# Kernel tuning notes

Measured on AMD Instinct MI355X. Metric: run time of the kernel, lower is better.

Reference implementation:

```python
import jax, jax.numpy as jnp
import numpy as np
from math import sqrt

N_HEADS = 16

def setup_inputs() -> dict:
    key = jax.random.key(0)
    ks = jax.random.split(key, 6)
    B, T, C = 4, 2048, 1024
    s = 0.02
    return {
        "X": jax.random.normal(ks[0], (B, T, C), jnp.float32),
        "Wq": jax.random.normal(ks[1], (C, C), jnp.float32) * s,
        "Wk": jax.random.normal(ks[2], (C, C), jnp.float32) * s,
        "Wv": jax.random.normal(ks[3], (C, C), jnp.float32) * s,
        "Wo": jax.random.normal(ks[4], (C, C), jnp.float32) * s,
        "bo": jnp.zeros((C,), jnp.float32),
    }

def reference(X, Wq, Wk, Wv, Wo, bo):
    B, T, C = X.shape
    H = N_HEADS
    D = C // H
    scale = sqrt(C / H)  # == sqrt(D)
    # Linear layers (torch Linear: y = x @ W.T), split into heads: [B,H,T,D]
    Q = (X @ Wq.T).reshape(B, T, H, D).transpose(0, 2, 1, 3)
    K = (X @ Wk.T).reshape(B, T, H, D).transpose(0, 2, 1, 3)
    V = (X @ Wv.T).reshape(B, T, H, D).transpose(0, 2, 1, 3)
    A = jnp.einsum("bhtd,bhsd->bhts", Q, K) / scale  # [B,H,T,T]
    causal = jnp.tril(jnp.ones((T, T), dtype=bool))
    A = jnp.where(causal, A, -jnp.inf)
    A = jax.nn.softmax(A, axis=-1)
    Y = jnp.einsum("bhts,bhsd->bhtd", A, V)  # [B,H,T,D]
    Y = Y.transpose(0, 2, 1, 3).reshape(B, T, C)
    return Y @ Wo.T + bo
```

## Files before the change

kernel.cpp:

```cpp
#include <hip/hip_runtime.h>
#include <hip/hip_bf16.h>
#include <stdint.h>


typedef unsigned short u16;
typedef __attribute__((ext_vector_type(8))) __bf16 bf16x8;
typedef __attribute__((ext_vector_type(4))) float  f32x4;
typedef __attribute__((ext_vector_type(4))) unsigned short u16x4;
typedef __attribute__((ext_vector_type(8))) unsigned short u16x8;
typedef __attribute__((ext_vector_type(4))) short s16x4;

#define B_  4
#define T_  2048
#define C_  1024
#define H_  16
#define D_  64
#define BT_ (B_ * T_)
#define NT_ 16

#define Q_SCALE 0.1803368801111204f

__device__ __forceinline__ u16 f32_to_bf16(float f) {
    unsigned int u = __float_as_uint(f);
    unsigned int r = (u + 0x7FFFu + ((u >> 16) & 1u)) >> 16;
    return (u16)r;
}

__device__ __forceinline__ unsigned int pk_bf16(float a, float b) {
    float2 f2; f2.x = a; f2.y = b;
    __hip_bfloat162 h = __float22bfloat162_rn(f2);
    return *(unsigned int*)&h;
}

__device__ __forceinline__ void async16(const void* g, void* lds) {
    __builtin_amdgcn_global_load_lds(
        (const __attribute__((address_space(1))) void*)g,
        (__attribute__((address_space(3))) void*)lds, 16, 0, 0);
}

__global__ void cast_all_kernel(const float* __restrict__ X,
                                const float* __restrict__ w0, const float* __restrict__ w1,
                                const float* __restrict__ w2, const float* __restrict__ w3,
                                u16* __restrict__ xo,
                                u16* __restrict__ o0, u16* __restrict__ o1,
                                u16* __restrict__ o2, u16* __restrict__ o3) {
    int id = blockIdx.x;
    const float* in; u16* out; int i;
    if (id < 8192) {
        in = X; out = xo; i = id * 256 + threadIdx.x;
    } else {
        int k = (id - 8192) >> 10;
        in  = (k == 0) ? w0 : (k == 1) ? w1 : (k == 2) ? w2 : w3;
        out = (k == 0) ? o0 : (k == 1) ? o1 : (k == 2) ? o2 : o3;
        i = ((id - 8192) & 1023) * 256 + threadIdx.x;
    }
    float4 v = ((const float4*)in)[i];
    u16x4 o;
    o[0] = f32_to_bf16(v.x); o[1] = f32_to_bf16(v.y);
    o[2] = f32_to_bf16(v.z); o[3] = f32_to_bf16(v.w);
    ((u16x4*)out)[i] = o;
}

#define QPHASE(CB, MH, NH, DOISSUE, G, GATE)                                      \
  {                                                                               \
    if ((NH) == 0) {                                                              \
      _Pragma("unroll")                                                           \
      for (int f = 0; f < 4; ++f) {                                               \
        _Pragma("unroll")                                                         \
        for (int ks = 0; ks < 2; ++ks)                                            \
          xf[f][ks] = *(const bf16x8*)((CB) + (MH) * 16384 + axoff[f][ks]);       \
      }                                                                           \
    }                                                                             \
    if ((MH) == 0) {                                                              \
      _Pragma("unroll")                                                           \
      for (int e = 0; e < 2; ++e) {                                               \
        _Pragma("unroll")                                                         \
        for (int ks = 0; ks < 2; ++ks)                                            \
          wf[NH][e][ks] = *(const bf16x8*)((CB) + (NH) * 16384 + bwoff[e][ks]);   \
      }                                                                           \
    }                                                                             \
    if (DOISSUE) issue_unit(G);                                                   \
    if ((GATE) == 4)      asm volatile("s_waitcnt vmcnt(4)" ::: "memory");        \
    else if ((GATE) == 2) asm volatile("s_waitcnt vmcnt(2)" ::: "memory");        \
    else if ((GATE) == 0) asm volatile("s_waitcnt vmcnt(0)" ::: "memory");        \
    __builtin_amdgcn_s_barrier();                                                 \
    asm volatile("" ::: "memory");                                                \
    __builtin_amdgcn_s_setprio(1);                                                \
    _Pragma("unroll")                                                             \
    for (int f = 0; f < 4; ++f) {                                                 \
      _Pragma("unroll")                                                           \
      for (int e = 0; e < 2; ++e) {                                               \
        f32x4 a_ = acc[(MH) * 4 + f][(NH) * 2 + e];                               \
        a_ = __builtin_amdgcn_mfma_f32_16x16x32_bf16(wf[NH][e][0], xf[f][0], a_, 0, 0, 0); \
        a_ = __builtin_amdgcn_mfma_f32_16x16x32_bf16(wf[NH][e][1], xf[f][1], a_, 0, 0, 0); \
        acc[(MH) * 4 + f][(NH) * 2 + e] = a_;                                     \
      }                                                                           \
    }                                                                             \
    __builtin_amdgcn_s_setprio(0);                                                \
    asm volatile("" ::: "memory");                                                \
    __builtin_amdgcn_s_barrier();                                                 \
    asm volatile("" ::: "memory");                                                \
  }

__device__ __forceinline__ void qkv256_core(const u16* __restrict__ Arow,
                                            const u16* __restrict__ Brow,
                                            char* lds, f32x4 (&acc)[8][4])
{
    int tid = threadIdx.x, lane = tid & 63, w = tid >> 6;
    int quad = lane >> 4, l15 = lane & 15;
    int wm = w >> 2, wn = w & 3;

    int gc = (((tid & 7) - (tid >> 3)) & 7) * 8;
    const u16* xsrc0 = Arow + (size_t)(tid >> 3) * C_ + gc;
    const u16* xsrc1 = xsrc0 + (size_t)64 * C_;
    const u16* wsrc0 = Brow + (size_t)(tid >> 3) * C_ + gc;
    const u16* wsrc1 = wsrc0 + (size_t)64 * C_;

    auto issue_unit = [&](int g) {
        int u = g & 3, kt = g >> 2;
        char* d = lds + ((kt & 1) << 16) + (u << 14) + (w << 10);
        size_t off = (size_t)(u & 1) * (128 * C_) + (size_t)kt * 64;
        const u16* s0 = (u < 2) ? xsrc0 : wsrc0;
        const u16* s1 = (u < 2) ? xsrc1 : wsrc1;
        async16(s0 + off, d);
        async16(s1 + off, d + 8192);
    };

    int axoff[4][2], bwoff[2][2];
#pragma unroll
    for (int f = 0; f < 4; ++f) {
        int r = wm * 64 + f * 16 + l15;
#pragma unroll
        for (int ks = 0; ks < 2; ++ks)
            axoff[f][ks] = r * 128 + (((ks * 4 + quad + r) & 7) << 4);
    }
#pragma unroll
    for (int e = 0; e < 2; ++e) {
        int r = wn * 32 + e * 16 + l15;
#pragma unroll
        for (int ks = 0; ks < 2; ++ks)
            bwoff[e][ks] = 32768 + r * 128 + (((ks * 4 + quad + r) & 7) << 4);
    }

    bf16x8 xf[4][2];
    bf16x8 wf[2][2][2];

    issue_unit(0); issue_unit(2); issue_unit(3); issue_unit(1);
    asm volatile("s_waitcnt vmcnt(4)" ::: "memory");
    __builtin_amdgcn_s_barrier();
    asm volatile("" ::: "memory");

    for (int t = 0; t < NT_ - 1; ++t) {
        char* cb = lds + ((t & 1) << 16);
        int g4 = (t + 1) << 2;
        QPHASE(cb, 0, 0, 1, g4 + 0, 4);
        QPHASE(cb, 0, 1, 1, g4 + 2, 4);
        QPHASE(cb, 1, 0, 1, g4 + 3, -1);
        QPHASE(cb, 1, 1, 1, g4 + 1, 4);
    }
    {
        char* cb = lds + 65536;
        QPHASE(cb, 0, 0, 0, 0, 2);
        QPHASE(cb, 0, 1, 0, 0, 0);
        QPHASE(cb, 1, 0, 0, 0, -1);
        QPHASE(cb, 1, 1, 0, 0, -1);
    }
}

__device__ __forceinline__ void qkv128v_core(const u16* __restrict__ Arow,
                                             const u16* __restrict__ Brow,
                                             char* lds, f32x4 (&acc)[4][4])
{
    int tid = threadIdx.x, lane = tid & 63, w = tid >> 6;
    int quad = lane >> 4, l15 = lane & 15;
    int wm = w >> 2, wn = w & 3;

    int gc = (((tid & 7) - (tid >> 3)) & 7) * 8;
    const u16* asrc  = Arow + (size_t)(tid >> 3) * C_ + gc;
    const u16* bsrc0 = Brow + (size_t)(tid >> 3) * C_ + gc;
    const u16* bsrc1 = bsrc0 + (size_t)64 * C_;

    auto issue3 = [&](int kt) {
        char* db = lds + ((kt & 1) << 16) + (w << 10);
        int ko = kt * 64;
        async16(asrc + ko,                       db);
        async16(asrc + ko + (size_t)64 * C_,     db + 8192);
        async16(bsrc0 + ko,                      db + 32768);
        async16(bsrc1 + ko,                      db + 32768 + 8192);
        async16(bsrc0 + ko + (size_t)128 * C_,   db + 49152);
        async16(bsrc1 + ko + (size_t)128 * C_,   db + 49152 + 8192);
    };

    int axoff[4][2], bwoff[2][2];
#pragma unroll
    for (int f = 0; f < 4; ++f) {
        int r = wm * 64 + f * 16 + l15;
#pragma unroll
        for (int ks = 0; ks < 2; ++ks)
            axoff[f][ks] = r * 128 + (((ks * 4 + quad + r) & 7) << 4);
    }
#pragma unroll
    for (int e = 0; e < 2; ++e) {
        int r = wn * 32 + e * 16 + l15;
#pragma unroll
        for (int ks = 0; ks < 2; ++ks)
            bwoff[e][ks] = 32768 + r * 128 + (((ks * 4 + quad + r) & 7) << 4);
    }

    bf16x8 xf[4][2], wf[2][2];

    issue3(0);

    for (int t = 0; t < NT_; ++t) {
        char* cb = lds + ((t & 1) << 16);
        if (t + 1 < NT_) issue3(t + 1);
        if (t == NT_ - 1) asm volatile("s_waitcnt vmcnt(0)" ::: "memory");
        else              asm volatile("s_waitcnt vmcnt(6)" ::: "memory");
        __builtin_amdgcn_s_barrier();
        asm volatile("" ::: "memory");

#pragma unroll
        for (int f = 0; f < 4; ++f)
#pragma unroll
            for (int ks = 0; ks < 2; ++ks)
                xf[f][ks] = *(const bf16x8*)(cb + axoff[f][ks]);
#pragma unroll
        for (int e = 0; e < 2; ++e)
#pragma unroll
            for (int ks = 0; ks < 2; ++ks)
                wf[e][ks] = *(const bf16x8*)(cb + bwoff[e][ks]);
        __builtin_amdgcn_s_setprio(1);
#pragma unroll
        for (int f = 0; f < 4; ++f)
#pragma unroll
            for (int e = 0; e < 2; ++e) {
                f32x4 a_ = acc[f][e];
                a_ = __builtin_amdgcn_mfma_f32_16x16x32_bf16(xf[f][0], wf[e][0], a_, 0, 0, 0);
                a_ = __builtin_amdgcn_mfma_f32_16x16x32_bf16(xf[f][1], wf[e][1], a_, 0, 0, 0);
                acc[f][e] = a_;
            }
        __builtin_amdgcn_s_setprio(0);

#pragma unroll
        for (int e = 0; e < 2; ++e)
#pragma unroll
            for (int ks = 0; ks < 2; ++ks)
                wf[e][ks] = *(const bf16x8*)(cb + 16384 + bwoff[e][ks]);
        __builtin_amdgcn_s_setprio(1);
#pragma unroll
        for (int f = 0; f < 4; ++f)
#pragma unroll
            for (int e = 0; e < 2; ++e) {
                f32x4 a_ = acc[f][2 + e];
                a_ = __builtin_amdgcn_mfma_f32_16x16x32_bf16(xf[f][0], wf[e][0], a_, 0, 0, 0);
                a_ = __builtin_amdgcn_mfma_f32_16x16x32_bf16(xf[f][1], wf[e][1], a_, 0, 0, 0);
                acc[f][2 + e] = a_;
            }
        __builtin_amdgcn_s_setprio(0);
        asm volatile("" ::: "memory");
        __builtin_amdgcn_s_barrier();
        asm volatile("" ::: "memory");
    }
}

__global__ __launch_bounds__(512, 2) void qkv_mix512(
    const u16* __restrict__ Xb, const u16* __restrict__ Wcat,
    u16* __restrict__ Qb, u16* __restrict__ Kb, u16* __restrict__ Vtb)
{
    __shared__ __attribute__((aligned(128))) char LDSRAW[131072];

    int id = blockIdx.x;
    int tid = threadIdx.x, lane = tid & 63, w = tid >> 6;
    int quad = lane >> 4, l15 = lane & 15;
    int wm = w >> 2, wn = w & 3;

    if (id < 256) {
        int ti = (id & 7) * 32 + (id >> 3);
        int bm = ti & 31, bn = ti >> 5;
        int m0 = bm * 256, chb = bn * 256;

        f32x4 acc[8][4];
        const f32x4 z4 = {0.f, 0.f, 0.f, 0.f};
#pragma unroll
        for (int i = 0; i < 8; ++i)
#pragma unroll
            for (int j = 0; j < 4; ++j) acc[i][j] = z4;

        qkv256_core(Xb + (size_t)m0 * C_, Wcat + (size_t)chb * C_, LDSRAW, acc);

#pragma unroll
        for (int mi = 0; mi < 8; ++mi) {
            size_t trow = (size_t)(m0 + (mi >> 2) * 128 + wm * 64 + (mi & 3) * 16 + l15) * C_;
#pragma unroll
            for (int nj = 0; nj < 4; ++nj) {
                int colb = chb + (nj >> 1) * 128 + wn * 32 + (nj & 1) * 16 + quad * 4;
                u16* OUT = (colb < 1024) ? Qb : Kb;
                float sc = (colb < 1024) ? Q_SCALE : 1.0f;
                u16x4 v;
#pragma unroll
                for (int rr = 0; rr < 4; ++rr) v[rr] = f32_to_bf16(acc[mi][nj][rr] * sc);
                *(u16x4*)&OUT[trow + (colb & 1023)] = v;
            }
        }
    } else {
        int id2 = id - 256;
        int hw = (id2 & 7) * 32 + (id2 >> 3);
        int vt = hw >> 6;
        int bm = (hw & 63) >> 1, half = hw & 1;
        int m0h = bm * 256 + half * 128;
        int chb = 2048 + vt * 256;

        f32x4 acc[4][4];
        const f32x4 z4 = {0.f, 0.f, 0.f, 0.f};
#pragma unroll
        for (int i = 0; i < 4; ++i)
#pragma unroll
            for (int j = 0; j < 4; ++j) acc[i][j] = z4;

        qkv128v_core(Xb + (size_t)m0h * C_, Wcat + (size_t)chb * C_, LDSRAW, acc);

#pragma unroll
        for (int mi = 0; mi < 4; ++mi) {
            int t0 = m0h + wm * 64 + mi * 16 + quad * 4;
            int b_ = t0 >> 11, tl = t0 & (T_ - 1);
#pragma unroll
            for (int nj = 0; nj < 4; ++nj) {
                int ch = chb + (nj >> 1) * 128 + wn * 32 + (nj & 1) * 16 + l15;
                int h = (ch >> 6) & 15, d = ch & 63;
                u16x4 v;
#pragma unroll
                for (int rr = 0; rr < 4; ++rr) v[rr] = f32_to_bf16(acc[mi][nj][rr]);
                *(u16x4*)&Vtb[((size_t)(b_ * H_ + h) * D_ + d) * T_ + tl] = v;
            }
        }
    }
}

#define RD8(CB, KS, FX, FW)                                                      \
    _Pragma("unroll") for (int i_ = 0; i_ < 4; ++i_) {                           \
        FX[i_] = *(const bf16x8*)((CB) + (KS) * 8192  + xoff[i_]);               \
        FW[i_] = *(const bf16x8*)((CB) + (KS) * 16384 + woff[i_]);               \
    }

#define PPH(ISSUE, GATE, FX, FW, ...)                                            \
  {                                                                              \
    ISSUE;                                                                       \
    if ((GATE) == 6)      asm volatile("s_waitcnt vmcnt(6)" ::: "memory");       \
    else if ((GATE) == 3) asm volatile("s_waitcnt vmcnt(3)" ::: "memory");       \
    else if ((GATE) == 0) asm volatile("s_waitcnt vmcnt(0)" ::: "memory");       \
    __builtin_amdgcn_s_barrier();                                                \
    asm volatile("" ::: "memory");                                               \
    __VA_ARGS__;                                                                 \
    __builtin_amdgcn_sched_barrier(0);                                           \
    __builtin_amdgcn_s_setprio(1);                                               \
    _Pragma("unroll") for (int i = 0; i < 4; ++i)                                \
      _Pragma("unroll") for (int j = 0; j < 4; ++j)                              \
        acc[i][j] = __builtin_amdgcn_mfma_f32_16x16x32_bf16(FW[j], FX[i], acc[i][j], 0, 0, 0); \
    __builtin_amdgcn_s_setprio(0);                                               \
    asm volatile("" ::: "memory");                                               \
    __builtin_amdgcn_s_barrier();                                                \
    asm volatile("" ::: "memory");                                               \
  }

__device__ __forceinline__ void gemm8p_core(const u16* __restrict__ Arow,
                                            const u16* __restrict__ Brow,
                                            char* lds, f32x4 (&acc)[4][4])
{
    int tid  = threadIdx.x;
    int lane = tid & 63, w = tid >> 6;
    int quad = lane >> 4, l15 = lane & 15;
    int wm = w >> 2, wn = w & 3;

    int r  = tid >> 2, s4 = tid & 3;
    int kg = ((s4 - (r >> 1)) & 3) * 8;
    const u16* xsrc  = Arow + (size_t)r * C_ + kg;
    const u16* wsrc0 = Brow + (size_t)r * C_ + kg;
    const u16* wsrc1 = Brow + (size_t)(128 + r) * C_ + kg;
    int wu = w << 10;

    int xoff[4], woff[4];
#pragma unroll
    for (int i = 0; i < 4; ++i) {
        int rx = wm * 64 + i * 16 + l15;
        xoff[i] = rx * 64 + (((rx >> 1) + quad) & 3) * 16;
        int rw = wn * 64 + i * 16 + l15;
        woff[i] = 16384 + rw * 64 + (((rw >> 1) + quad) & 3) * 16;
    }

    auto issue_group = [&](int g) {
        int db = (g >> 1) & 1, ks = g & 1;
        int koff = (g >> 1) * 64 + ks * 32;
        char* ldb = lds + db * 49152;
        async16(xsrc  + koff, ldb + ks * 8192 + wu);
        async16(wsrc0 + koff, ldb + 16384 + ks * 16384 + wu);
        async16(wsrc1 + koff, ldb + 16384 + ks * 16384 + 8192 + wu);
    };

    bf16x8 fAx[4], fAw[4], fBx[4], fBw[4];

    issue_group(0); issue_group(1); issue_group(2);
    asm volatile("s_waitcnt vmcnt(6)" ::: "memory");
    __builtin_amdgcn_s_barrier();
    asm volatile("" ::: "memory");
    RD8(lds, 0, fAx, fAw);

    for (int t = 0; t < NT_ - 1; ++t) {
        char* cb  = lds + (t & 1) * 49152;
        char* cbn = lds + ((t + 1) & 1) * 49152;
        PPH({ issue_group(2 * t + 3); }, 6, fAx, fAw, { RD8(cb, 1, fBx, fBw); });
        if (t < NT_ - 2) {
            PPH({ issue_group(2 * t + 4); }, 6, fBx, fBw, { RD8(cbn, 0, fAx, fAw); });
        } else {
            PPH({}, 3, fBx, fBw, { RD8(cbn, 0, fAx, fAw); });
        }
    }
    {
        char* cb = lds + ((NT_ - 1) & 1) * 49152;
        PPH({}, 0, fAx, fAw, { RD8(cb, 1, fBx, fBw); });
        PPH({}, -1, fBx, fBw, {});
    }
}

__global__ __launch_bounds__(256, 4) void attn_kernel(
    const u16* __restrict__ Qb, const u16* __restrict__ Kb,
    const u16* __restrict__ Vtb, u16* __restrict__ Yb)
{
    __shared__ u16 SMA[16384];
    u16* Ks0 = SMA;
    u16* Ks1 = SMA + 4096;
    u16* Vs0 = SMA + 8192;
    u16* Vs1 = SMA + 12288;

    int id = blockIdx.x;
    int bh = id & 63;
    int jj = id >> 6;

    int tid = threadIdx.x, lane = tid & 63, w = tid >> 6;
    int quad = lane >> 4, l15 = lane & 15;
    int b = bh >> 4, h = bh & 15;

    int koff0[4], koff1[4], voff[4][4];
#pragma unroll
    for (int sblk = 0; sblk < 4; ++sblk) {
        int sr = sblk * 16 + l15;
        koff0[sblk] = (sr * 64 + ((quad + sr) & 7) * 8) * 2;
        koff1[sblk] = (sr * 64 + ((4 + quad + sr) & 7) * 8) * 2;
    }
#pragma unroll
    for (int n = 0; n < 4; ++n)
#pragma unroll
        for (int sblk = 0; sblk < 4; ++sblk) {
            int dr = n * 16 + l15;
            voff[n][sblk] = (dr * 64 + ((sblk * 2 + (quad >> 1) + dr) & 7) * 8 + (quad & 1) * 4) * 2;
        }

    int cA = tid, cB = tid + 256;
    int sA = cA >> 3, sB = cB >> 3;
    int offA = (((cA & 7) - sA) & 7) * 8;
    int offB = (((cB & 7) - sB) & 7) * 8;
    const u16* Kbase = Kb + (size_t)(b * T_) * C_ + h * 64;
    const u16* Vbase = Vtb + (size_t)bh * D_ * T_;
    int ldsb0 = (w * 64) * 16, ldsb1 = (256 + w * 64) * 16;

    const s16x4 ones = { (short)0x3F80, (short)0x3F80, (short)0x3F80, (short)0x3F80 };
    const f32x4 z4 = {0.f, 0.f, 0.f, 0.f};

    int qts[2] = { jj, 31 - jj };

    for (int pass = 0; pass < 2; ++pass) {
        int qt = qts[pass];
        int qbase = qt * 64;

        if (pass) __syncthreads();

        bf16x8 qf0, qf1;
        {
            const u16* q0 = Qb + ((size_t)(b * T_ + qbase + w * 16 + l15)) * C_ + h * 64;
            qf0 = *(const bf16x8*)(q0 + quad * 8);
            qf1 = *(const bf16x8*)(q0 + 32 + quad * 8);
        }

        f32x4 o_acc[4];
        f32x4 l_acc = z4;
#pragma unroll
        for (int n = 0; n < 4; ++n) o_acc[n] = z4;

        const int nst = qt + 1;

        const u16* kgpA = Kbase + (size_t)sA * C_ + offA;
        const u16* kgpB = Kbase + (size_t)sB * C_ + offB;
        const u16* vgpA = Vbase + sA * T_ + offA;
        const u16* vgpB = Vbase + sB * T_ + offB;

        async16(kgpA, (char*)Ks0 + ldsb0);
        async16(kgpB, (char*)Ks0 + ldsb1);
        async16(vgpA, (char*)Vs0 + ldsb0);
        async16(vgpB, (char*)Vs0 + ldsb1);
        kgpA += 64 * C_; kgpB += 64 * C_; vgpA += 64; vgpB += 64;

        auto tile_body = [&](int st, const u16* K_, const u16* V_, char* Kpf, char* Vpf) {
            __syncthreads();
            if (st + 1 < nst) {
                async16(kgpA, Kpf + ldsb0);
                async16(kgpB, Kpf + ldsb1);
                async16(vgpA, Vpf + ldsb0);
                async16(vgpB, Vpf + ldsb1);
            }
            kgpA += 64 * C_; kgpB += 64 * C_; vgpA += 64; vgpB += 64;

            f32x4 sv[4];
#pragma unroll
            for (int sblk = 0; sblk < 4; ++sblk) {
                bf16x8 k0 = *(const bf16x8*)((const char*)K_ + koff0[sblk]);
                bf16x8 k1 = *(const bf16x8*)((const char*)K_ + koff1[sblk]);
                f32x4 t0 = __builtin_amdgcn_mfma_f32_16x16x32_bf16(k0, qf0, z4, 0, 0, 0);
                sv[sblk] = __builtin_amdgcn_mfma_f32_16x16x32_bf16(k1, qf1, t0, 0, 0, 0);
            }

            if (st == qt) {
                int tl = w * 16 + l15;
#pragma unroll
                for (int sblk = 0; sblk < 4; ++sblk)
#pragma unroll
                    for (int r = 0; r < 4; ++r)
                        if (sblk * 16 + quad * 4 + r > tl) sv[sblk][r] = -1e30f;
            }

            s16x4 pfrag[4];
#pragma unroll
            for (int sblk = 0; sblk < 4; ++sblk) {
#pragma unroll
                for (int r = 0; r < 4; ++r)
                    sv[sblk][r] = __builtin_amdgcn_exp2f(sv[sblk][r]);
                uint2 pk;
                pk.x = pk_bf16(sv[sblk][0], sv[sblk][1]);
                pk.y = pk_bf16(sv[sblk][2], sv[sblk][3]);
                pfrag[sblk] = *(s16x4*)&pk;
                l_acc = __builtin_amdgcn_mfma_f32_16x16x16bf16_1k(ones, pfrag[sblk], l_acc, 0, 0, 0);
            }

#pragma unroll
            for (int n = 0; n < 4; ++n)
#pragma unroll
                for (int sblk = 0; sblk < 4; ++sblk) {
                    s16x4 va = *(const s16x4*)((const char*)V_ + voff[n][sblk]);
                    o_acc[n] = __builtin_amdgcn_mfma_f32_16x16x16bf16_1k(va, pfrag[sblk], o_acc[n], 0, 0, 0);
                }
        };

        for (int st = 0; st < nst; st += 2) {
            tile_body(st, Ks0, Vs0, (char*)Ks1, (char*)Vs1);
            if (st + 1 < nst)
                tile_body(st + 1, Ks1, Vs1, (char*)Ks0, (char*)Vs0);
        }

        __syncthreads();
        u16* PW = SMA + w * 1152;
        {
            float inv = 1.0f / l_acc[0];
#pragma unroll
            for (int n = 0; n < 4; ++n) {
                uint2 pk;
                pk.x = pk_bf16(o_acc[n][0] * inv, o_acc[n][1] * inv);
                pk.y = pk_bf16(o_acc[n][2] * inv, o_acc[n][3] * inv);
                *(u16x4*)&PW[l15 * 72 + n * 16 + quad * 4] = *(u16x4*)&pk;
            }
        }
        asm volatile("s_waitcnt lgkmcnt(0)" ::: "memory");
#pragma unroll
        for (int st = 0; st < 2; ++st) {
            int tr = st * 8 + (lane >> 3);
            int d8 = (lane & 7) * 8;
            u16x8 v = *(u16x8*)&PW[tr * 72 + d8];
            *(u16x8*)&Yb[(size_t)(b * T_ + qbase + w * 16 + tr) * C_ + h * 64 + d8] = v;
        }
    }
}

__global__ __launch_bounds__(512, 2) void proj_gemm8(
    const u16* __restrict__ Yb, const u16* __restrict__ Wob,
    const float* __restrict__ bo, float* __restrict__ out)
{
    __shared__ __attribute__((aligned(128))) char LDSRAW[98304];

    int id = blockIdx.x;
    int wg = (id & 7) * 32 + (id >> 3);
    int bm = wg >> 2, bn = wg & 3;
    int m0 = bm * 128, n0 = bn * 256;

    f32x4 acc[4][4];
    const f32x4 z4 = {0.f, 0.f, 0.f, 0.f};
#pragma unroll
    for (int i = 0; i < 4; ++i)
#pragma unroll
        for (int j = 0; j < 4; ++j) acc[i][j] = z4;

    gemm8p_core(Yb + (size_t)m0 * C_, Wob + (size_t)n0 * C_, LDSRAW, acc);

    int tid = threadIdx.x, lane = tid & 63, w = tid >> 6;
    int quad = lane >> 4, l15 = lane & 15;
    int wm = w >> 2, wn = w & 3;

#pragma unroll
    for (int j = 0; j < 4; ++j) {
        int ch = n0 + wn * 64 + j * 16 + quad * 4;
        f32x4 bv = *(const f32x4*)&bo[ch];
#pragma unroll
        for (int i = 0; i < 4; ++i) {
            int t = m0 + wm * 64 + i * 16 + l15;
            f32x4 v = acc[i][j] + bv;
            *(f32x4*)&out[(size_t)t * C_ + ch] = v;
        }
    }
}

extern "C" void kernel_launch(void* const* d_in, const int* in_sizes, int n_in,
                              void* d_out, int out_size, void* d_ws, size_t ws_size,
                              hipStream_t stream) {
    const float* X  = (const float*)d_in[0];
    const float* Wq = (const float*)d_in[1];
    const float* Wk = (const float*)d_in[2];
    const float* Wv = (const float*)d_in[3];
    const float* Wo = (const float*)d_in[4];
    const float* bo = (const float*)d_in[5];

    char* ws = (char*)d_ws;
    u16* Xb  = (u16*)(ws);
    u16* Wqb = (u16*)(ws + (16u << 20));
    u16* Wkb = (u16*)(ws + (18u << 20));
    u16* Wvb = (u16*)(ws + (20u << 20));
    u16* Wob = (u16*)(ws + (22u << 20));
    u16* Qb  = (u16*)(ws + (24u << 20));
    u16* Kb  = (u16*)(ws + (40u << 20));
    u16* Vtb = (u16*)(ws + (56u << 20));
    u16* Yb  = (u16*)(ws + (72u << 20));

    cast_all_kernel<<<dim3(8192 + 4 * 1024), 256, 0, stream>>>(
        X, Wq, Wk, Wv, Wo, Xb, Wqb, Wkb, Wvb, Wob);

    qkv_mix512<<<dim3(512), 512, 0, stream>>>(Xb, Wqb, Qb, Kb, Vtb);
    attn_kernel<<<dim3(1024), 256, 0, stream>>>(Qb, Kb, Vtb, Yb);
    proj_gemm8<<<dim3(256), 512, 0, stream>>>(Yb, Wob, bo, (float*)d_out);
}
```

Before: 230.4 us.

## Share K/V tile loads between both query tiles in one causal attention pass

Instead of two sequential passes over K/V for the paired query tiles jj and 31-jj, the kernel now streams K/V once, up to the longer tile's range, and computes both query tiles against each loaded tile while the shorter one is still in range. This removes the redundant reloading of the shared K/V prefix and one pass's barriers and prologue. The cost is double the live accumulators and Q fragments, which raises register pressure under launch bounds of 256 threads with 4 blocks. LDS offsets are also simplified to a base plus constant strides to free registers.

```diff
diff --git a/kernel.cpp b/kernel.cpp
--- a/kernel.cpp
+++ b/kernel.cpp
@@ -434,30 +434,25 @@
     int id = blockIdx.x;
     int bh = id & 63;
     int jj = id >> 6;
+    int qtA = jj, qtB = 31 - jj;
+    const int nstA = qtA + 1;
+    const int nstB = qtB + 1;
 
     int tid = threadIdx.x, lane = tid & 63, w = tid >> 6;
     int quad = lane >> 4, l15 = lane & 15;
     int b = bh >> 4, h = bh & 15;
 
-    int koff0[4], koff1[4], voff[4][4];
-#pragma unroll
-    for (int sblk = 0; sblk < 4; ++sblk) {
-        int sr = sblk * 16 + l15;
-        koff0[sblk] = (sr * 64 + ((quad + sr) & 7) * 8) * 2;
-        koff1[sblk] = (sr * 64 + ((4 + quad + sr) & 7) * 8) * 2;
-    }
-#pragma unroll
-    for (int n = 0; n < 4; ++n)
-#pragma unroll
-        for (int sblk = 0; sblk < 4; ++sblk) {
-            int dr = n * 16 + l15;
-            voff[n][sblk] = (dr * 64 + ((sblk * 2 + (quad >> 1) + dr) & 7) * 8 + (quad & 1) * 4) * 2;
-        }
-
-    int cA = tid, cB = tid + 256;
-    int sA = cA >> 3, sB = cB >> 3;
-    int offA = (((cA & 7) - sA) & 7) * 8;
-    int offB = (((cB & 7) - sB) & 7) * 8;
+    int koffb0 = l15 * 128 + ((quad + l15) & 7) * 16;
+    int koffb1 = l15 * 128 + ((4 + quad + l15) & 7) * 16;
+    int voffb[4];
+#pragma unroll
+    for (int sblk = 0; sblk < 4; ++sblk)
+        voffb[sblk] = l15 * 128 + ((sblk * 2 + (quad >> 1) + l15) & 7) * 16 + (quad & 1) * 8;
+
+    int cA_ = tid, cB_ = tid + 256;
+    int sA = cA_ >> 3, sB = cB_ >> 3;
+    int offA = (((cA_ & 7) - sA) & 7) * 8;
+    int offB = (((cB_ & 7) - sB) & 7) * 8;
     const u16* Kbase = Kb + (size_t)(b * T_) * C_ + h * 64;
     const u16* Vbase = Vtb + (size_t)bh * D_ * T_;
     int ldsb0 = (w * 64) * 16, ldsb1 = (256 + w * 64) * 16;
@@ -465,59 +460,52 @@
     const s16x4 ones = { (short)0x3F80, (short)0x3F80, (short)0x3F80, (short)0x3F80 };
     const f32x4 z4 = {0.f, 0.f, 0.f, 0.f};
 
-    int qts[2] = { jj, 31 - jj };
-
-    for (int pass = 0; pass < 2; ++pass) {
-        int qt = qts[pass];
-        int qbase = qt * 64;
-
-        if (pass) __syncthreads();
-
-        bf16x8 qf0, qf1;
+    bf16x8 qfA0, qfA1, qfB0, qfB1;
+    {
+        const u16* qA = Qb + ((size_t)(b * T_ + qtA * 64 + w * 16 + l15)) * C_ + h * 64;
+        qfA0 = *(const bf16x8*)(qA + quad * 8);
+        qfA1 = *(const bf16x8*)(qA + 32 + quad * 8);
+        const u16* qB = Qb + ((size_t)(b * T_ + qtB * 64 + w * 16 + l15)) * C_ + h * 64;
+        qfB0 = *(const bf16x8*)(qB + quad * 8);
+        qfB1 = *(const bf16x8*)(qB + 32 + quad * 8);
+    }
+
+    f32x4 oA[4], oB[4];
+    f32x4 lA = z4, lB = z4;
+#pragma unroll
+    for (int n = 0; n < 4; ++n) { oA[n] = z4; oB[n] = z4; }
+
+    const u16* kgpA = Kbase + (size_t)sA * C_ + offA;
+    const u16* kgpB = Kbase + (size_t)sB * C_ + offB;
+    const u16* vgpA = Vbase + sA * T_ + offA;
+    const u16* vgpB = Vbase + sB * T_ + offB;
+
+    async16(kgpA, (char*)Ks0 + ldsb0);
+    async16(kgpB, (char*)Ks0 + ldsb1);
+    async16(vgpA, (char*)Vs0 + ldsb0);
+    async16(vgpB, (char*)Vs0 + ldsb1);
+    kgpA += 64 * C_; kgpB += 64 * C_; vgpA += 64; vgpB += 64;
+
+    auto tile_body = [&](int st, const u16* K_, const u16* V_, char* Kpf, char* Vpf) {
+        __syncthreads();
+        if (st + 1 < nstB) {
+            async16(kgpA, Kpf + ldsb0);
+            async16(kgpB, Kpf + ldsb1);
+            async16(vgpA, Vpf + ldsb0);
+            async16(vgpB, Vpf + ldsb1);
+        }
+        kgpA += 64 * C_; kgpB += 64 * C_; vgpA += 64; vgpB += 64;
+
         {
-            const u16* q0 = Qb + ((size_t)(b * T_ + qbase + w * 16 + l15)) * C_ + h * 64;
-            qf0 = *(const bf16x8*)(q0 + quad * 8);
-            qf1 = *(const bf16x8*)(q0 + 32 + quad * 8);
-        }
-
-        f32x4 o_acc[4];
-        f32x4 l_acc = z4;
-#pragma unroll
-        for (int n = 0; n < 4; ++n) o_acc[n] = z4;
-
-        const int nst = qt + 1;
-
-        const u16* kgpA = Kbase + (size_t)sA * C_ + offA;
-        const u16* kgpB = Kbase + (size_t)sB * C_ + offB;
-        const u16* vgpA = Vbase + sA * T_ + offA;
-        const u16* vgpB = Vbase + sB * T_ + offB;
-
-        async16(kgpA, (char*)Ks0 + ldsb0);
-        async16(kgpB, (char*)Ks0 + ldsb1);
-        async16(vgpA, (char*)Vs0 + ldsb0);
-        async16(vgpB, (char*)Vs0 + ldsb1);
-        kgpA += 64 * C_; kgpB += 64 * C_; vgpA += 64; vgpB += 64;
-
-        auto tile_body = [&](int st, const u16* K_, const u16* V_, char* Kpf, char* Vpf) {
-            __syncthreads();
-            if (st + 1 < nst) {
-                async16(kgpA, Kpf + ldsb0);
-                async16(kgpB, Kpf + ldsb1);
-                async16(vgpA, Vpf + ldsb0);
-                async16(vgpB, Vpf + ldsb1);
-            }
-            kgpA += 64 * C_; kgpB += 64 * C_; vgpA += 64; vgpB += 64;
-
             f32x4 sv[4];
 #pragma unroll
             for (int sblk = 0; sblk < 4; ++sblk) {
-                bf16x8 k0 = *(const bf16x8*)((const char*)K_ + koff0[sblk]);
-                bf16x8 k1 = *(const bf16x8*)((const char*)K_ + koff1[sblk]);
-                f32x4 t0 = __builtin_amdgcn_mfma_f32_16x16x32_bf16(k0, qf0, z4, 0, 0, 0);
-                sv[sblk] = __builtin_amdgcn_mfma_f32_16x16x32_bf16(k1, qf1, t0, 0, 0, 0);
-            }
-
-            if (st == qt) {
+                bf16x8 k0 = *(const bf16x8*)((const char*)K_ + sblk * 2048 + koffb0);
+                bf16x8 k1 = *(const bf16x8*)((const char*)K_ + sblk * 2048 + koffb1);
+                f32x4 t0 = __builtin_amdgcn_mfma_f32_16x16x32_bf16(k0, qfB0, z4, 0, 0, 0);
+                sv[sblk] = __builtin_amdgcn_mfma_f32_16x16x32_bf16(k1, qfB1, t0, 0, 0, 0);
+            }
+            if (st == qtB) {
                 int tl = w * 16 + l15;
 #pragma unroll
                 for (int sblk = 0; sblk < 4; ++sblk)
@@ -525,7 +513,6 @@
                     for (int r = 0; r < 4; ++r)
                         if (sblk * 16 + quad * 4 + r > tl) sv[sblk][r] = -1e30f;
             }
-
             s16x4 pfrag[4];
 #pragma unroll
             for (int sblk = 0; sblk < 4; ++sblk) {
@@ -536,44 +523,100 @@
                 pk.x = pk_bf16(sv[sblk][0], sv[sblk][1]);
                 pk.y = pk_bf16(sv[sblk][2], sv[sblk][3]);
                 pfrag[sblk] = *(s16x4*)&pk;
-                l_acc = __builtin_amdgcn_mfma_f32_16x16x16bf16_1k(ones, pfrag[sblk], l_acc, 0, 0, 0);
-            }
-
+                lB = __builtin_amdgcn_mfma_f32_16x16x16bf16_1k(ones, pfrag[sblk], lB, 0, 0, 0);
+            }
 #pragma unroll
             for (int n = 0; n < 4; ++n)
 #pragma unroll
                 for (int sblk = 0; sblk < 4; ++sblk) {
-                    s16x4 va = *(const s16x4*)((const char*)V_ + voff[n][sblk]);
-                    o_acc[n] = __builtin_amdgcn_mfma_f32_16x16x16bf16_1k(va, pfrag[sblk], o_acc[n], 0, 0, 0);
+                    s16x4 va = *(const s16x4*)((const char*)V_ + n * 2048 + voffb[sblk]);
+                    oB[n] = __builtin_amdgcn_mfma_f32_16x16x16bf16_1k(va, pfrag[sblk], oB[n], 0, 0, 0);
                 }
-        };
-
-        for (int st = 0; st < nst; st += 2) {
-            tile_body(st, Ks0, Vs0, (char*)Ks1, (char*)Vs1);
-            if (st + 1 < nst)
-                tile_body(st + 1, Ks1, Vs1, (char*)Ks0, (char*)Vs0);
-        }
-
-        __syncthreads();
-        u16* PW = SMA + w * 1152;
-        {
-            float inv = 1.0f / l_acc[0];
-#pragma unroll
-            for (int n = 0; n < 4; ++n) {
+        }
+
+        if (st < nstA) {
+            f32x4 sv[4];
+#pragma unroll
+            for (int sblk = 0; sblk < 4; ++sblk) {
+                bf16x8 k0 = *(const bf16x8*)((const char*)K_ + sblk * 2048 + koffb0);
+                bf16x8 k1 = *(const bf16x8*)((const char*)K_ + sblk * 2048 + koffb1);
+                f32x4 t0 = __builtin_amdgcn_mfma_f32_16x16x32_bf16(k0, qfA0, z4, 0, 0, 0);
+                sv[sblk] = __builtin_amdgcn_mfma_f32_16x16x32_bf16(k1, qfA1, t0, 0, 0, 0);
+            }
+            if (st == qtA) {
+                int tl = w * 16 + l15;
+#pragma unroll
+                for (int sblk = 0; sblk < 4; ++sblk)
+#pragma unroll
+                    for (int r = 0; r < 4; ++r)
+                        if (sblk * 16 + quad * 4 + r > tl) sv[sblk][r] = -1e30f;
+            }
+            s16x4 pfrag[4];
+#pragma unroll
+            for (int sblk = 0; sblk < 4; ++sblk) {
+#pragma unroll
+                for (int r = 0; r < 4; ++r)
+                    sv[sblk][r] = __builtin_amdgcn_exp2f(sv[sblk][r]);
                 uint2 pk;
-                pk.x = pk_bf16(o_acc[n][0] * inv, o_acc[n][1] * inv);
-                pk.y = pk_bf16(o_acc[n][2] * inv, o_acc[n][3] * inv);
-                *(u16x4*)&PW[l15 * 72 + n * 16 + quad * 4] = *(u16x4*)&pk;
-            }
-        }
-        asm volatile("s_waitcnt lgkmcnt(0)" ::: "memory");
-#pragma unroll
-        for (int st = 0; st < 2; ++st) {
-            int tr = st * 8 + (lane >> 3);
-            int d8 = (lane & 7) * 8;
-            u16x8 v = *(u16x8*)&PW[tr * 72 + d8];
-            *(u16x8*)&Yb[(size_t)(b * T_ + qbase + w * 16 + tr) * C_ + h * 64 + d8] = v;
-        }
+                pk.x = pk_bf16(sv[sblk][0], sv[sblk][1]);
+                pk.y = pk_bf16(sv[sblk][2], sv[sblk][3]);
+                pfrag[sblk] = *(s16x4*)&pk;
+                lA = __builtin_amdgcn_mfma_f32_16x16x16bf16_1k(ones, pfrag[sblk], lA, 0, 0, 0);
+            }
+#pragma unroll
+            for (int n = 0; n < 4; ++n)
+#pragma unroll
+                for (int sblk = 0; sblk < 4; ++sblk) {
+                    s16x4 va = *(const s16x4*)((const char*)V_ + n * 2048 + voffb[sblk]);
+                    oA[n] = __builtin_amdgcn_mfma_f32_16x16x16bf16_1k(va, pfrag[sblk], oA[n], 0, 0, 0);
+                }
+        }
+    };
+
+    for (int st = 0; st < nstB; st += 2) {
+        tile_body(st, Ks0, Vs0, (char*)Ks1, (char*)Vs1);
+        if (st + 1 < nstB)
+            tile_body(st + 1, Ks1, Vs1, (char*)Ks0, (char*)Vs0);
+    }
+
+    __syncthreads();
+    u16* PW = SMA + w * 1152;
+    {
+        float inv = 1.0f / lA[0];
+#pragma unroll
+        for (int n = 0; n < 4; ++n) {
+            uint2 pk;
+            pk.x = pk_bf16(oA[n][0] * inv, oA[n][1] * inv);
+            pk.y = pk_bf16(oA[n][2] * inv, oA[n][3] * inv);
+            *(u16x4*)&PW[l15 * 72 + n * 16 + quad * 4] = *(u16x4*)&pk;
+        }
+    }
+    asm volatile("s_waitcnt lgkmcnt(0)" ::: "memory");
+#pragma unroll
+    for (int st = 0; st < 2; ++st) {
+        int tr = st * 8 + (lane >> 3);
+        int d8 = (lane & 7) * 8;
+        u16x8 v = *(u16x8*)&PW[tr * 72 + d8];
+        *(u16x8*)&Yb[(size_t)(b * T_ + qtA * 64 + w * 16 + tr) * C_ + h * 64 + d8] = v;
+    }
+    asm volatile("s_waitcnt lgkmcnt(0)" ::: "memory");
+    {
+        float inv = 1.0f / lB[0];
+#pragma unroll
+        for (int n = 0; n < 4; ++n) {
+            uint2 pk;
+            pk.x = pk_bf16(oB[n][0] * inv, oB[n][1] * inv);
+            pk.y = pk_bf16(oB[n][2] * inv, oB[n][3] * inv);
+            *(u16x4*)&PW[l15 * 72 + n * 16 + quad * 4] = *(u16x4*)&pk;
+        }
+    }
+    asm volatile("s_waitcnt lgkmcnt(0)" ::: "memory");
+#pragma unroll
+    for (int st = 0; st < 2; ++st) {
+        int tr = st * 8 + (lane >> 3);
+        int d8 = (lane & 7) * 8;
+        u16x8 v = *(u16x8*)&PW[tr * 72 + d8];
+        *(u16x8*)&Yb[(size_t)(b * T_ + qtB * 64 + w * 16 + tr) * C_ + h * 64 + d8] = v;
     }
 }
 
```

New measurement: 277.0 us. +20.2%, slower.
